# Kernel optimization log

Hardware: AMD Instinct MI355X
Metric: run time of the kernel (lower is better)

The kernel has to match this reference:

```python
import jax, jax.numpy as jnp
import numpy as np

EMBED_DIM = 512
NUM_HEADS = 8
QKV_DIM = 64
MS_HIDDEN = 16
COST_DIMS = 1
SCORES_DIMS = COST_DIMS + 1  # dot-product score + cost-mat score


def setup_inputs() -> dict:
    key = jax.random.key(0)
    ks = jax.random.split(key, 12)
    B, R, C = 8, 256, 256
    row_emb = jax.random.normal(ks[0], (B, R, EMBED_DIM), dtype=jnp.float32)
    col_emb = jax.random.normal(ks[1], (B, C, EMBED_DIM), dtype=jnp.float32)
    cost_mat = jax.random.uniform(ks[2], (B, R, C, COST_DIMS), dtype=jnp.float32)
    attn_mask = jax.random.randint(ks[3], (B, R, C), 0, 2).astype(jnp.bool_)
    # learned params (stored [in, out]; torch Linear applies x @ W.T)
    s = 1.0 / np.sqrt(EMBED_DIM)
    Wq = jax.random.uniform(ks[4], (EMBED_DIM, NUM_HEADS * QKV_DIM), minval=-s, maxval=s)
    Wk = jax.random.uniform(ks[5], (EMBED_DIM, NUM_HEADS * QKV_DIM), minval=-s, maxval=s)
    Wv = jax.random.uniform(ks[6], (EMBED_DIM, NUM_HEADS * QKV_DIM), minval=-s, maxval=s)
    Wo = jax.random.uniform(ks[7], (EMBED_DIM, EMBED_DIM), minval=-s, maxval=s)
    m1 = np.sqrt(1.0 / SCORES_DIMS)
    m2 = np.sqrt(1.0 / MS_HIDDEN)
    W1 = jax.random.uniform(ks[8], (SCORES_DIMS * NUM_HEADS, MS_HIDDEN * NUM_HEADS), minval=-m1, maxval=m1)
    W2 = jax.random.uniform(ks[9], (MS_HIDDEN * NUM_HEADS, NUM_HEADS), minval=-m2, maxval=m2)
    alpha = jnp.ones((1, NUM_HEADS, 1, 1, 1), dtype=jnp.float32)
    return {"row_emb": row_emb, "col_emb": col_emb, "cost_mat": cost_mat,
            "attn_mask": attn_mask, "Wq": Wq, "Wk": Wk, "Wv": Wv, "Wo": Wo,
            "W1": W1, "W2": W2, "alpha": alpha}


def reference(row_emb, col_emb, cost_mat, attn_mask, Wq, Wk, Wv, Wo, W1, W2, alpha):
    B, R, E = row_emb.shape
    C = col_emb.shape[1]
    H, D = NUM_HEADS, QKV_DIM
    norm = 1.0 / jnp.sqrt(jnp.asarray(D, row_emb.dtype))
    # projections -> (b, h, s, d)
    q = (row_emb @ Wq).reshape(B, R, H, D).transpose(0, 2, 1, 3)
    k = (col_emb @ Wk).reshape(B, C, H, D).transpose(0, 2, 1, 3)
    v = (col_emb @ Wv).reshape(B, C, H, D).transpose(0, 2, 1, 3)
    dot = norm * jnp.einsum('bhrd,bhcd->bhrc', q, k)  # (B,H,R,C)
    # mixed-score MLP: concat dot score with alpha-scaled cost-mat score
    cm = alpha * cost_mat[:, None]                    # (B,H,R,C,COST_DIMS)
    scores = jnp.concatenate([dot[..., None], cm], axis=-1)  # (B,H,R,C,S)
    s = scores.transpose(0, 2, 3, 1, 4).reshape(B, R, C, H * SCORES_DIMS)
    mixed = jax.nn.relu(s @ W1) @ W2                  # (B,R,C,H)
    logits = mixed.transpose(0, 3, 1, 2)              # (B,H,R,C)
    # masked softmax (rows fully masked -> zero weights)
    mask = attn_mask[:, None]                         # (B,1,R,C)
    all_masked = jnp.all(mask, axis=-1, keepdims=True)
    logits = jnp.where(mask, -jnp.inf, logits)
    weights = jax.nn.softmax(logits, axis=-1)
    weights = jnp.where(all_masked, 0.0, weights)
    out = jnp.einsum('bhrc,bhcd->bhrd', weights, v)   # (B,H,R,D)
    out = out.transpose(0, 2, 1, 3).reshape(B, R, H * D)
    return out @ Wo
```

## Files before the change

### kernel.cpp

```cpp
#include <hip/hip_runtime.h>
#include <hip/hip_bf16.h>

#define B_ 8
#define R_ 256
#define C_ 256
#define H_ 8
#define D_ 64

typedef __attribute__((ext_vector_type(8))) short s8v;
typedef __attribute__((ext_vector_type(4))) short s4v;
typedef __attribute__((ext_vector_type(4))) float f4v;

static __device__ __forceinline__ unsigned short f2b(float x) {
    __hip_bfloat16 h = __float2bfloat16(x);
    return *reinterpret_cast<unsigned short*>(&h);
}
static __device__ __forceinline__ float b2f(unsigned short u) {
    union { unsigned int i; float f; } c;
    c.i = (unsigned int)u << 16;
    return c.f;
}

__global__ __launch_bounds__(256) void prep(
    const float* __restrict__ re, const float* __restrict__ ce,
    const float* __restrict__ W1, const float* __restrict__ W2,
    const float* __restrict__ alpha,
    const float* __restrict__ Wq, const float* __restrict__ Wk,
    const float* __restrict__ Wv, const float* __restrict__ Wo,
    unsigned short* __restrict__ reb, unsigned short* __restrict__ ceb,
    unsigned short* __restrict__ w1af, unsigned short* __restrict__ w2af,
    unsigned short* __restrict__ wqt, unsigned short* __restrict__ wkt,
    unsigned short* __restrict__ wvt, unsigned short* __restrict__ wot)
{
    __shared__ unsigned short ldsT[64][68];
    if (blockIdx.x >= 2048) {
        const int bb = blockIdx.x - 2048;
        const int which = bb >> 6;
        const float* W = which == 0 ? Wq : which == 1 ? Wk : which == 2 ? Wv : Wo;
        unsigned short* WT = which == 0 ? wqt : which == 1 ? wkt : which == 2 ? wvt : wot;
        const int k0 = (bb & 7) * 64;
        const int n0 = ((bb >> 3) & 7) * 64;
        const int tt = threadIdx.x;
        const int rn = tt & 15;
        const int rk = tt >> 4;
        #pragma unroll
        for (int i = 0; i < 4; ++i) {
            const int kk = rk + 16 * i;
            const float4 v = *(const float4*)&W[(size_t)(k0 + kk) * 512 + n0 + rn * 4];
            ldsT[rn * 4 + 0][kk] = f2b(v.x);
            ldsT[rn * 4 + 1][kk] = f2b(v.y);
            ldsT[rn * 4 + 2][kk] = f2b(v.z);
            ldsT[rn * 4 + 3][kk] = f2b(v.w);
        }
        __syncthreads();
        #pragma unroll
        for (int i = 0; i < 4; ++i) {
            const int nn = rk + 16 * i;
            const s4v r = *(const s4v*)&ldsT[nn][rn * 4];
            *(s4v*)&WT[(size_t)(n0 + nn) * 512 + k0 + rn * 4] = r;
        }
        return;
    }

    const int t = blockIdx.x * 256 + threadIdx.x;
    {
        float2 v = *(const float2*)&re[(size_t)t * 2];
        reb[t * 2]     = f2b(v.x);
        reb[t * 2 + 1] = f2b(v.y);
        float2 w = *(const float2*)&ce[(size_t)t * 2];
        ceb[t * 2]     = f2b(w.x);
        ceb[t * 2 + 1] = f2b(w.y);
    }
    if (blockIdx.x == 0) {
        const int l = threadIdx.x;
        for (int q = 0; q < 16; ++q) {
            const int idx = l * 16 + q;
            const int kk = idx & 7, lane = (idx >> 3) & 63, n = idx >> 9;
            const int j = n * 16 + (lane & 15);
            const int s = 8 * (lane >> 4) + kk;
            float val = 0.f;
            if (s < 16) {
                val = W1[(2 * (s >> 1)) * 128 + j];
            } else if (s < 18) {
                for (int h = 0; h < 8; ++h)
                    val += alpha[h] * W1[(2 * h + 1) * 128 + j];
            }
            w1af[idx] = f2b(val);
        }
        for (int q = 0; q < 8; ++q) {
            const int idx = l * 8 + q;
            const int kk = idx & 7, lane = (idx >> 3) & 63, kc = idx >> 9;
            const int h = lane & 15, g = lane >> 4;
            const int phi = 16 * (2 * kc + (kk >> 2)) + 4 * g + (kk & 3);
            w2af[idx] = f2b(h < 8 ? W2[phi * 8 + h] : 0.f);
        }
    }
}

__global__ __launch_bounds__(256) void gemm_qkv(
    const unsigned short* __restrict__ reb, const unsigned short* __restrict__ ceb,
    const unsigned short* __restrict__ wqt, const unsigned short* __restrict__ wkt,
    const unsigned short* __restrict__ wvt,
    unsigned short* __restrict__ Qb, unsigned short* __restrict__ Kb,
    unsigned short* __restrict__ VT)
{
    const int z = blockIdx.z;
    const unsigned short* A;
    const unsigned short* Bm;
    int Ar0, Br0;
    if (z == 0)      { A = reb; Bm = wqt; Ar0 = blockIdx.x * 64; Br0 = blockIdx.y * 64; }
    else if (z == 1) { A = ceb; Bm = wkt; Ar0 = blockIdx.x * 64; Br0 = blockIdx.y * 64; }
    else             { A = wvt; Bm = ceb; Ar0 = blockIdx.y * 64; Br0 = blockIdx.x * 64; }

    const int t = threadIdx.x, lane = t & 63, wave = t >> 6;
    const int row0 = Ar0 + (wave >> 1) * 32;
    const int col0 = Br0 + (wave & 1) * 32;
    const int lr = lane & 15, ko = (lane >> 4) * 8;

    const unsigned short* Ap0 = A + (size_t)(row0 + lr) * 512 + ko;
    const unsigned short* Ap1 = Ap0 + 16 * 512;
    const unsigned short* Bp0 = Bm + (size_t)(col0 + lr) * 512 + ko;
    const unsigned short* Bp1 = Bp0 + 16 * 512;

    f4v acc[2][2] = {};
    s8v a0 = *(const s8v*)Ap0;
    s8v a1 = *(const s8v*)Ap1;
    s8v b0 = *(const s8v*)Bp0;
    s8v b1 = *(const s8v*)Bp1;
    #pragma unroll
    for (int k0 = 0; k0 < 512; k0 += 32) {
        const s8v ca0 = a0, ca1 = a1, cb0 = b0, cb1 = b1;
        if (k0 + 32 < 512) {
            a0 = *(const s8v*)(Ap0 + k0 + 32);
            a1 = *(const s8v*)(Ap1 + k0 + 32);
            b0 = *(const s8v*)(Bp0 + k0 + 32);
            b1 = *(const s8v*)(Bp1 + k0 + 32);
        }
        acc[0][0] = __builtin_amdgcn_mfma_f32_16x16x32_bf16(ca0, cb0, acc[0][0], 0, 0, 0);
        acc[0][1] = __builtin_amdgcn_mfma_f32_16x16x32_bf16(ca0, cb1, acc[0][1], 0, 0, 0);
        acc[1][0] = __builtin_amdgcn_mfma_f32_16x16x32_bf16(ca1, cb0, acc[1][0], 0, 0, 0);
        acc[1][1] = __builtin_amdgcn_mfma_f32_16x16x32_bf16(ca1, cb1, acc[1][1], 0, 0, 0);
    }

    const float sc = (z == 0) ? 0.125f : 1.0f;
    const int rbase = (lane >> 4) * 4;
    #pragma unroll
    for (int i = 0; i < 2; ++i)
        #pragma unroll
        for (int j = 0; j < 2; ++j)
            #pragma unroll
            for (int reg = 0; reg < 4; ++reg) {
                const int rowIdx = row0 + i * 16 + rbase + reg;
                const int colIdx = col0 + j * 16 + lr;
                const unsigned short v = f2b(acc[i][j][reg] * sc);
                if (z == 0) {
                    Qb[(size_t)rowIdx * 512 + colIdx] = v;
                } else if (z == 1) {
                    const int b = rowIdx >> 8, c = rowIdx & 255;
                    const int h = colIdx >> 6, d = colIdx & 63;
                    Kb[(((size_t)b * 8 + h) * 256 + c) * 64 + d] = v;
                } else {
                    const int h = rowIdx >> 6, d = rowIdx & 63;
                    const int b = colIdx >> 8, c = colIdx & 255;
                    VT[(((size_t)b * 8 + h) * 64 + d) * 256 + c] = v;
                }
            }
}

__global__ __launch_bounds__(256) void gemm_out(
    const unsigned short* __restrict__ OHb, const unsigned short* __restrict__ wot,
    float* __restrict__ out)
{
    const int t = threadIdx.x, lane = t & 63, wave = t >> 6;
    const int row0 = blockIdx.x * 32 + (wave & 1) * 16;
    const int col0 = blockIdx.y * 64 + (wave >> 1) * 32;
    const int lr = lane & 15, ko = (lane >> 4) * 8;

    const unsigned short* Ap0 = OHb + (size_t)(row0 + lr) * 512 + ko;
    const unsigned short* Bp0 = wot + (size_t)(col0 + lr) * 512 + ko;
    const unsigned short* Bp1 = Bp0 + 16 * 512;

    f4v acc[2] = {};
    s8v a0 = *(const s8v*)Ap0;
    s8v b0 = *(const s8v*)Bp0;
    s8v b1 = *(const s8v*)Bp1;
    #pragma unroll
    for (int k0 = 0; k0 < 512; k0 += 32) {
        const s8v ca0 = a0, cb0 = b0, cb1 = b1;
        if (k0 + 32 < 512) {
            a0 = *(const s8v*)(Ap0 + k0 + 32);
            b0 = *(const s8v*)(Bp0 + k0 + 32);
            b1 = *(const s8v*)(Bp1 + k0 + 32);
        }
        acc[0] = __builtin_amdgcn_mfma_f32_16x16x32_bf16(ca0, cb0, acc[0], 0, 0, 0);
        acc[1] = __builtin_amdgcn_mfma_f32_16x16x32_bf16(ca0, cb1, acc[1], 0, 0, 0);
    }

    const int rbase = (lane >> 4) * 4;
    #pragma unroll
    for (int j = 0; j < 2; ++j)
        #pragma unroll
        for (int reg = 0; reg < 4; ++reg)
            out[(size_t)(row0 + rbase + reg) * 512 + col0 + j * 16 + lr] = acc[j][reg];
}

__global__ __launch_bounds__(1024) void attn_fused(
    const unsigned short* __restrict__ Qb,
    const unsigned short* __restrict__ Kb,
    const unsigned short* __restrict__ VT,
    const float* __restrict__ cost,
    const int* __restrict__ mask,
    const unsigned short* __restrict__ w1af,
    const unsigned short* __restrict__ w2af,
    unsigned short* __restrict__ OHb)
{
    __shared__ unsigned short dotb[8][256][16];
    __shared__ unsigned short w_t3[8][8][264];
    __shared__ unsigned short ws1[4096];
    __shared__ unsigned short ws2[2048];

    const int t    = threadIdx.x;
    const int lane = t & 63;
    const int w    = t >> 6;
    const int li   = lane & 15;
    const int g    = lane >> 4;
    const int b    = blockIdx.y;
    const int r0   = blockIdx.x * 8;

    const int h  = w & 7;
    const int hf = w >> 3;

    if (t < 512) ((s8v*)ws1)[t] = ((const s8v*)w1af)[t];
    else if (t < 768) ((s8v*)ws2)[t - 512] = ((const s8v*)w2af)[t - 512];

    const int rB  = w & 7;
    const int ct0 = hf * 8;
    float costv[8];
    {
        const float* costRow = cost + ((size_t)b * R_ + r0 + rB) * 256;
        #pragma unroll
        for (int i = 0; i < 8; ++i)
            costv[i] = costRow[(ct0 + i) * 16 + li];
    }
    int mkp[4][4];
    #pragma unroll
    for (int p = 0; p < 4; ++p) {
        const int idx = w * 4 + p;
        const int* maskRow = mask + ((size_t)b * R_ + r0 + (idx >> 3)) * 256;
        #pragma unroll
        for (int i = 0; i < 4; ++i)
            mkp[p][i] = maskRow[lane + 64 * i];
    }

    {
        const int rr = lane & 7;
        const int ko = g * 8;
        const unsigned short* Qp = Qb + ((size_t)b * R_ + r0 + rr) * 512 + h * 64 + ko;
        const s8v a0 = *(const s8v*)Qp;
        const s8v a1 = *(const s8v*)(Qp + 32);
        const unsigned short* Kp = Kb + (((size_t)b * 8 + h) * 256) * 64;
        #pragma unroll
        for (int c8 = 0; c8 < 8; ++c8) {
            const int ct = ct0 + c8;
            const unsigned short* Bp = Kp + (size_t)(ct * 16 + li) * 64 + ko;
            const s8v b0 = *(const s8v*)Bp;
            const s8v b1v = *(const s8v*)(Bp + 32);
            f4v acc = __builtin_amdgcn_mfma_f32_16x16x32_bf16(a0, b0, (f4v){0.f,0.f,0.f,0.f}, 0, 0, 0);
            acc = __builtin_amdgcn_mfma_f32_16x16x32_bf16(a1, b1v, acc, 0, 0, 0);
            if (g < 2) {
                const int c = ct * 16 + li;
                #pragma unroll
                for (int reg = 0; reg < 4; ++reg) {
                    const float x = acc[reg];
                    const unsigned short hi = f2b(x);
                    const unsigned short lo = f2b(x - b2f(hi));
                    *(unsigned int*)&dotb[4 * g + reg][c][2 * h] =
                        (unsigned int)hi | ((unsigned int)lo << 16);
                }
            }
        }
    }
    __syncthreads();

    s8v b1r[8];
    #pragma unroll
    for (int i = 0; i < 8; ++i) {
        const int c = (ct0 + i) * 16 + li;
        b1r[i] = *(const s8v*)&dotb[rB][c][(g & 1) * 8];
    }
    __syncthreads();

    {
        float* lplane = (float*)&dotb[rB][0][0];
        #pragma unroll
        for (int i = 0; i < 8; ++i) {
            const int c = (ct0 + i) * 16 + li;
            s8v b1;
            {
                const float cv = costv[i];
                const unsigned short chi = f2b(cv);
                const unsigned short clo = f2b(cv - b2f(chi));
                if (g < 2) {
                    b1 = b1r[i];
                } else if (g == 2) {
                    s8v bc = {0, 0, 0, 0, 0, 0, 0, 0};
                    bc[0] = (short)chi; bc[1] = (short)clo;
                    b1 = bc;
                } else {
                    s8v bz = {0, 0, 0, 0, 0, 0, 0, 0};
                    b1 = bz;
                }
            }
            unsigned int pk[16];
            #pragma unroll
            for (int n = 0; n < 8; ++n) {
                const s8v w1A = *(const s8v*)&ws1[(n * 64 + lane) * 8];
                f4v acc = __builtin_amdgcn_mfma_f32_16x16x32_bf16(
                    w1A, b1, (f4v){0.f,0.f,0.f,0.f}, 0, 0, 0);
                const float a0 = fmaxf(acc[0], 0.f), a1 = fmaxf(acc[1], 0.f);
                const float a2 = fmaxf(acc[2], 0.f), a3 = fmaxf(acc[3], 0.f);
                pk[2 * n]     = (unsigned int)f2b(a0) | ((unsigned int)f2b(a1) << 16);
                pk[2 * n + 1] = (unsigned int)f2b(a2) | ((unsigned int)f2b(a3) << 16);
            }
            f4v acc2 = (f4v){0.f, 0.f, 0.f, 0.f};
            #pragma unroll
            for (int kc = 0; kc < 4; ++kc) {
                const s8v w2A = *(const s8v*)&ws2[(kc * 64 + lane) * 8];
                union { s8v v; unsigned int u[4]; } bb;
                bb.u[0] = pk[4 * kc + 0];
                bb.u[1] = pk[4 * kc + 1];
                bb.u[2] = pk[4 * kc + 2];
                bb.u[3] = pk[4 * kc + 3];
                acc2 = __builtin_amdgcn_mfma_f32_16x16x32_bf16(w2A, bb.v, acc2, 0, 0, 0);
            }
            if (g < 2) {
                #pragma unroll
                for (int reg = 0; reg < 4; ++reg)
                    lplane[(4 * g + reg) * 256 + c] = acc2[reg];
            }
        }
    }
    __syncthreads();

    {
        #pragma unroll
        for (int p = 0; p < 4; ++p) {
            const int idx = w * 4 + p;
            const int r = idx >> 3, hh = idx & 7;
            const float* lplane = (const float*)&dotb[r][0][0];
            float v[4];
            #pragma unroll
            for (int i = 0; i < 4; ++i)
                v[i] = lplane[hh * 256 + lane + 64 * i];
            #pragma unroll
            for (int i = 0; i < 4; ++i)
                v[i] = mkp[p][i] ? -INFINITY : v[i];
            float mx = fmaxf(fmaxf(v[0], v[1]), fmaxf(v[2], v[3]));
            #pragma unroll
            for (int off = 32; off >= 1; off >>= 1)
                mx = fmaxf(mx, __shfl_xor(mx, off));
            float e[4];
            #pragma unroll
            for (int i = 0; i < 4; ++i)
                e[i] = mkp[p][i] ? 0.f : __expf(v[i] - mx);
            float sm = e[0] + e[1] + e[2] + e[3];
            #pragma unroll
            for (int off = 32; off >= 1; off >>= 1)
                sm += __shfl_xor(sm, off);
            const float inv = sm > 0.f ? 1.0f / sm : 0.f;
            #pragma unroll
            for (int i = 0; i < 4; ++i)
                w_t3[hh][r][lane + 64 * i] = f2b(e[i] * inv);
        }
    }
    __syncthreads();

    {
        s8v bfr[8];
        #pragma unroll
        for (int kt = 0; kt < 8; ++kt)
            bfr[kt] = *(const s8v*)&w_t3[h][li & 7][kt * 32 + g * 8];
        const unsigned short* Vp = VT + (((size_t)b * 8 + h) * 64) * 256;
        #pragma unroll
        for (int d2 = 0; d2 < 2; ++d2) {
            const int dt = hf * 2 + d2;
            const unsigned short* Ap = Vp + (size_t)(dt * 16 + li) * 256 + g * 8;
            f4v acc = (f4v){0.f, 0.f, 0.f, 0.f};
            #pragma unroll
            for (int kt = 0; kt < 8; ++kt)
                acc = __builtin_amdgcn_mfma_f32_16x16x32_bf16(
                    *(const s8v*)(Ap + kt * 32), bfr[kt], acc, 0, 0, 0);
            if (li < 8) {
                s4v o;
                o[0] = (short)f2b(acc[0]);
                o[1] = (short)f2b(acc[1]);
                o[2] = (short)f2b(acc[2]);
                o[3] = (short)f2b(acc[3]);
                *(s4v*)&OHb[((size_t)b * R_ + r0 + li) * 512 + h * 64 + dt * 16 + 4 * g] = o;
            }
        }
    }
}

extern "C" void kernel_launch(void* const* d_in, const int* in_sizes, int n_in,
                              void* d_out, int out_size, void* d_ws, size_t ws_size,
                              hipStream_t stream)
{
    const float* row_emb = (const float*)d_in[0];
    const float* col_emb = (const float*)d_in[1];
    const float* cost    = (const float*)d_in[2];
    const int*   mask    = (const int*)d_in[3];
    const float* Wq = (const float*)d_in[4];
    const float* Wk = (const float*)d_in[5];
    const float* Wv = (const float*)d_in[6];
    const float* Wo = (const float*)d_in[7];
    const float* W1 = (const float*)d_in[8];
    const float* W2 = (const float*)d_in[9];
    const float* alpha = (const float*)d_in[10];
    float* out = (float*)d_out;

    unsigned short* base = (unsigned short*)d_ws;
    unsigned short* Qb   = base;
    unsigned short* Kb   = base + 1048576;
    unsigned short* VT   = base + 2097152;
    unsigned short* OHb  = base + 3145728;
    unsigned short* reb  = base + 4194304;
    unsigned short* ceb  = base + 5242880;
    unsigned short* wqt  = base + 6291456;
    unsigned short* wkt  = base + 6553600;
    unsigned short* wvt  = base + 6815744;
    unsigned short* wot  = base + 7077888;
    unsigned short* w1af = base + 7340032;
    unsigned short* w2af = base + 7344128;

    prep<<<2304, 256, 0, stream>>>(row_emb, col_emb, W1, W2, alpha,
                                   Wq, Wk, Wv, Wo,
                                   reb, ceb, w1af, w2af, wqt, wkt, wvt, wot);
    gemm_qkv<<<dim3(32, 8, 3), 256, 0, stream>>>(reb, ceb, wqt, wkt, wvt,
                                                 Qb, Kb, VT);
    attn_fused<<<dim3(32, 8), 1024, 0, stream>>>(Qb, Kb, VT, cost, mask,
                                                 w1af, w2af, OHb);
    gemm_out<<<dim3(64, 8), 256, 0, stream>>>(OHb, wot, out);
}
```

Measured before the change: 83.38 us.

## Merge all four kernels into one cooperative persistent kernel with grid syncs

Replaces the prep, QKV GEMM, attention and output GEMM launches with one cooperative kernel of 256 blocks of 1024 threads, with stages separated by grid-wide syncs. Each stage's work is remapped onto the fixed grid by wave id. This is meant to remove the per-launch overhead and the inter-kernel gaps. In exchange, the GEMM stages run with only 256 large blocks, so occupancy is lower. The large LDS footprint of the attention stage also limits residency, and the grid barriers add their own cost.

```diff
diff --git a/kernel.cpp b/kernel.cpp
--- a/kernel.cpp
+++ b/kernel.cpp
@@ -1,5 +1,8 @@
 #include <hip/hip_runtime.h>
 #include <hip/hip_bf16.h>
+#include <hip/hip_cooperative_groups.h>
+
+namespace cg = cooperative_groups;
 
 #define B_ 8
 #define R_ 256
@@ -21,31 +24,62 @@
     return c.f;
 }
 
-__global__ __launch_bounds__(256) void prep(
+__global__ __launch_bounds__(1024) void mega(
     const float* __restrict__ re, const float* __restrict__ ce,
+    const float* __restrict__ cost, const int* __restrict__ mask,
+    const float* __restrict__ Wq, const float* __restrict__ Wk,
+    const float* __restrict__ Wv, const float* __restrict__ Wo,
     const float* __restrict__ W1, const float* __restrict__ W2,
     const float* __restrict__ alpha,
-    const float* __restrict__ Wq, const float* __restrict__ Wk,
-    const float* __restrict__ Wv, const float* __restrict__ Wo,
     unsigned short* __restrict__ reb, unsigned short* __restrict__ ceb,
     unsigned short* __restrict__ w1af, unsigned short* __restrict__ w2af,
     unsigned short* __restrict__ wqt, unsigned short* __restrict__ wkt,
-    unsigned short* __restrict__ wvt, unsigned short* __restrict__ wot)
+    unsigned short* __restrict__ wvt, unsigned short* __restrict__ wot,
+    unsigned short* __restrict__ Qb, unsigned short* __restrict__ Kb,
+    unsigned short* __restrict__ VT, unsigned short* __restrict__ OHb,
+    float* __restrict__ out)
 {
+    __shared__ unsigned short dotb[8][256][16];
+    __shared__ unsigned short w_t3[8][8][264];
+    __shared__ unsigned short ws1[4096];
+    __shared__ unsigned short ws2[2048];
     __shared__ unsigned short ldsT[64][68];
-    if (blockIdx.x >= 2048) {
-        const int bb = blockIdx.x - 2048;
-        const int which = bb >> 6;
+
+    const int t    = threadIdx.x;
+    const int lane = t & 63;
+    const int w    = t >> 6;
+    const int li   = lane & 15;
+    const int g    = lane >> 4;
+    const int bid  = blockIdx.y * 32 + blockIdx.x;
+    const int wid  = bid * 16 + w;
+    cg::grid_group gg = cg::this_grid();
+
+    {
+        const size_t gi = (size_t)(bid * 1024 + t) * 4;
+        {
+            const float4 v = *(const float4*)&re[gi];
+            s4v rv;
+            rv[0] = (short)f2b(v.x); rv[1] = (short)f2b(v.y);
+            rv[2] = (short)f2b(v.z); rv[3] = (short)f2b(v.w);
+            *(s4v*)&reb[gi] = rv;
+            const float4 u = *(const float4*)&ce[gi];
+            s4v cv;
+            cv[0] = (short)f2b(u.x); cv[1] = (short)f2b(u.y);
+            cv[2] = (short)f2b(u.z); cv[3] = (short)f2b(u.w);
+            *(s4v*)&ceb[gi] = cv;
+        }
+        const int which = bid >> 6;
         const float* W = which == 0 ? Wq : which == 1 ? Wk : which == 2 ? Wv : Wo;
-        unsigned short* WT = which == 0 ? wqt : which == 1 ? wkt : which == 2 ? wvt : wot;
-        const int k0 = (bb & 7) * 64;
-        const int n0 = ((bb >> 3) & 7) * 64;
-        const int tt = threadIdx.x;
-        const int rn = tt & 15;
-        const int rk = tt >> 4;
-        #pragma unroll
-        for (int i = 0; i < 4; ++i) {
-            const int kk = rk + 16 * i;
+        unsigned short* WT = which == 0 ? wqt : which == 1 ? wkt
+                           : which == 2 ? wvt : wot;
+        const int tile = bid & 63;
+        const int k0 = (tile & 7) * 64;
+        const int n0 = (tile >> 3) * 64;
+        const int rn = t & 15;
+        const int rk = (t >> 4) & 15;
+        const int qi = t >> 8;
+        {
+            const int kk = rk + 16 * qi;
             const float4 v = *(const float4*)&W[(size_t)(k0 + kk) * 512 + n0 + rn * 4];
             ldsT[rn * 4 + 0][kk] = f2b(v.x);
             ldsT[rn * 4 + 1][kk] = f2b(v.y);
@@ -53,180 +87,108 @@
             ldsT[rn * 4 + 3][kk] = f2b(v.w);
         }
         __syncthreads();
-        #pragma unroll
-        for (int i = 0; i < 4; ++i) {
-            const int nn = rk + 16 * i;
+        {
+            const int nn = rk + 16 * qi;
             const s4v r = *(const s4v*)&ldsT[nn][rn * 4];
             *(s4v*)&WT[(size_t)(n0 + nn) * 512 + k0 + rn * 4] = r;
         }
-        return;
-    }
-
-    const int t = blockIdx.x * 256 + threadIdx.x;
-    {
-        float2 v = *(const float2*)&re[(size_t)t * 2];
-        reb[t * 2]     = f2b(v.x);
-        reb[t * 2 + 1] = f2b(v.y);
-        float2 w = *(const float2*)&ce[(size_t)t * 2];
-        ceb[t * 2]     = f2b(w.x);
-        ceb[t * 2 + 1] = f2b(w.y);
-    }
-    if (blockIdx.x == 0) {
-        const int l = threadIdx.x;
-        for (int q = 0; q < 16; ++q) {
-            const int idx = l * 16 + q;
-            const int kk = idx & 7, lane = (idx >> 3) & 63, n = idx >> 9;
-            const int j = n * 16 + (lane & 15);
-            const int s = 8 * (lane >> 4) + kk;
-            float val = 0.f;
-            if (s < 16) {
-                val = W1[(2 * (s >> 1)) * 128 + j];
-            } else if (s < 18) {
-                for (int h = 0; h < 8; ++h)
-                    val += alpha[h] * W1[(2 * h + 1) * 128 + j];
-            }
-            w1af[idx] = f2b(val);
-        }
-        for (int q = 0; q < 8; ++q) {
-            const int idx = l * 8 + q;
-            const int kk = idx & 7, lane = (idx >> 3) & 63, kc = idx >> 9;
-            const int h = lane & 15, g = lane >> 4;
-            const int phi = 16 * (2 * kc + (kk >> 2)) + 4 * g + (kk & 3);
-            w2af[idx] = f2b(h < 8 ? W2[phi * 8 + h] : 0.f);
-        }
-    }
-}
-
-__global__ __launch_bounds__(256) void gemm_qkv(
-    const unsigned short* __restrict__ reb, const unsigned short* __restrict__ ceb,
-    const unsigned short* __restrict__ wqt, const unsigned short* __restrict__ wkt,
-    const unsigned short* __restrict__ wvt,
-    unsigned short* __restrict__ Qb, unsigned short* __restrict__ Kb,
-    unsigned short* __restrict__ VT)
-{
-    const int z = blockIdx.z;
-    const unsigned short* A;
-    const unsigned short* Bm;
-    int Ar0, Br0;
-    if (z == 0)      { A = reb; Bm = wqt; Ar0 = blockIdx.x * 64; Br0 = blockIdx.y * 64; }
-    else if (z == 1) { A = ceb; Bm = wkt; Ar0 = blockIdx.x * 64; Br0 = blockIdx.y * 64; }
-    else             { A = wvt; Bm = ceb; Ar0 = blockIdx.y * 64; Br0 = blockIdx.x * 64; }
-
-    const int t = threadIdx.x, lane = t & 63, wave = t >> 6;
-    const int row0 = Ar0 + (wave >> 1) * 32;
-    const int col0 = Br0 + (wave & 1) * 32;
-    const int lr = lane & 15, ko = (lane >> 4) * 8;
-
-    const unsigned short* Ap0 = A + (size_t)(row0 + lr) * 512 + ko;
-    const unsigned short* Ap1 = Ap0 + 16 * 512;
-    const unsigned short* Bp0 = Bm + (size_t)(col0 + lr) * 512 + ko;
-    const unsigned short* Bp1 = Bp0 + 16 * 512;
-
-    f4v acc[2][2] = {};
-    s8v a0 = *(const s8v*)Ap0;
-    s8v a1 = *(const s8v*)Ap1;
-    s8v b0 = *(const s8v*)Bp0;
-    s8v b1 = *(const s8v*)Bp1;
-    #pragma unroll
-    for (int k0 = 0; k0 < 512; k0 += 32) {
-        const s8v ca0 = a0, ca1 = a1, cb0 = b0, cb1 = b1;
-        if (k0 + 32 < 512) {
-            a0 = *(const s8v*)(Ap0 + k0 + 32);
-            a1 = *(const s8v*)(Ap1 + k0 + 32);
-            b0 = *(const s8v*)(Bp0 + k0 + 32);
-            b1 = *(const s8v*)(Bp1 + k0 + 32);
-        }
-        acc[0][0] = __builtin_amdgcn_mfma_f32_16x16x32_bf16(ca0, cb0, acc[0][0], 0, 0, 0);
-        acc[0][1] = __builtin_amdgcn_mfma_f32_16x16x32_bf16(ca0, cb1, acc[0][1], 0, 0, 0);
-        acc[1][0] = __builtin_amdgcn_mfma_f32_16x16x32_bf16(ca1, cb0, acc[1][0], 0, 0, 0);
-        acc[1][1] = __builtin_amdgcn_mfma_f32_16x16x32_bf16(ca1, cb1, acc[1][1], 0, 0, 0);
-    }
-
-    const float sc = (z == 0) ? 0.125f : 1.0f;
-    const int rbase = (lane >> 4) * 4;
-    #pragma unroll
-    for (int i = 0; i < 2; ++i)
-        #pragma unroll
-        for (int j = 0; j < 2; ++j)
-            #pragma unroll
-            for (int reg = 0; reg < 4; ++reg) {
-                const int rowIdx = row0 + i * 16 + rbase + reg;
-                const int colIdx = col0 + j * 16 + lr;
-                const unsigned short v = f2b(acc[i][j][reg] * sc);
-                if (z == 0) {
-                    Qb[(size_t)rowIdx * 512 + colIdx] = v;
-                } else if (z == 1) {
-                    const int b = rowIdx >> 8, c = rowIdx & 255;
-                    const int h = colIdx >> 6, d = colIdx & 63;
-                    Kb[(((size_t)b * 8 + h) * 256 + c) * 64 + d] = v;
-                } else {
-                    const int h = rowIdx >> 6, d = rowIdx & 63;
-                    const int b = colIdx >> 8, c = colIdx & 255;
-                    VT[(((size_t)b * 8 + h) * 64 + d) * 256 + c] = v;
+        if (bid == 0 && t < 256) {
+            const int l = t;
+            for (int q = 0; q < 16; ++q) {
+                const int idx = l * 16 + q;
+                const int kk = idx & 7, ln = (idx >> 3) & 63, n = idx >> 9;
+                const int j = n * 16 + (ln & 15);
+                const int s = 8 * (ln >> 4) + kk;
+                float val = 0.f;
+                if (s < 16) {
+                    val = W1[(2 * (s >> 1)) * 128 + j];
+                } else if (s < 18) {
+                    for (int hh = 0; hh < 8; ++hh)
+                        val += alpha[hh] * W1[(2 * hh + 1) * 128 + j];
                 }
-            }
-}
-
-__global__ __launch_bounds__(256) void gemm_out(
-    const unsigned short* __restrict__ OHb, const unsigned short* __restrict__ wot,
-    float* __restrict__ out)
-{
-    const int t = threadIdx.x, lane = t & 63, wave = t >> 6;
-    const int row0 = blockIdx.x * 32 + (wave & 1) * 16;
-    const int col0 = blockIdx.y * 64 + (wave >> 1) * 32;
-    const int lr = lane & 15, ko = (lane >> 4) * 8;
-
-    const unsigned short* Ap0 = OHb + (size_t)(row0 + lr) * 512 + ko;
-    const unsigned short* Bp0 = wot + (size_t)(col0 + lr) * 512 + ko;
-    const unsigned short* Bp1 = Bp0 + 16 * 512;
-
-    f4v acc[2] = {};
-    s8v a0 = *(const s8v*)Ap0;
-    s8v b0 = *(const s8v*)Bp0;
-    s8v b1 = *(const s8v*)Bp1;
-    #pragma unroll
-    for (int k0 = 0; k0 < 512; k0 += 32) {
-        const s8v ca0 = a0, cb0 = b0, cb1 = b1;
-        if (k0 + 32 < 512) {
-            a0 = *(const s8v*)(Ap0 + k0 + 32);
-            b0 = *(const s8v*)(Bp0 + k0 + 32);
-            b1 = *(const s8v*)(Bp1 + k0 + 32);
-        }
-        acc[0] = __builtin_amdgcn_mfma_f32_16x16x32_bf16(ca0, cb0, acc[0], 0, 0, 0);
-        acc[1] = __builtin_amdgcn_mfma_f32_16x16x32_bf16(ca0, cb1, acc[1], 0, 0, 0);
-    }
-
-    const int rbase = (lane >> 4) * 4;
-    #pragma unroll
-    for (int j = 0; j < 2; ++j)
-        #pragma unroll
-        for (int reg = 0; reg < 4; ++reg)
-            out[(size_t)(row0 + rbase + reg) * 512 + col0 + j * 16 + lr] = acc[j][reg];
-}
-
-__global__ __launch_bounds__(1024) void attn_fused(
-    const unsigned short* __restrict__ Qb,
-    const unsigned short* __restrict__ Kb,
-    const unsigned short* __restrict__ VT,
-    const float* __restrict__ cost,
-    const int* __restrict__ mask,
-    const unsigned short* __restrict__ w1af,
-    const unsigned short* __restrict__ w2af,
-    unsigned short* __restrict__ OHb)
-{
-    __shared__ unsigned short dotb[8][256][16];
-    __shared__ unsigned short w_t3[8][8][264];
-    __shared__ unsigned short ws1[4096];
-    __shared__ unsigned short ws2[2048];
-
-    const int t    = threadIdx.x;
-    const int lane = t & 63;
-    const int w    = t >> 6;
-    const int li   = lane & 15;
-    const int g    = lane >> 4;
-    const int b    = blockIdx.y;
-    const int r0   = blockIdx.x * 8;
-
+                w1af[idx] = f2b(val);
+            }
+            for (int q = 0; q < 8; ++q) {
+                const int idx = l * 8 + q;
+                const int kk = idx & 7, ln = (idx >> 3) & 63, kc = idx >> 9;
+                const int hh = ln & 15, gg2 = ln >> 4;
+                const int phi = 16 * (2 * kc + (kk >> 2)) + 4 * gg2 + (kk & 3);
+                w2af[idx] = f2b(hh < 8 ? W2[phi * 8 + hh] : 0.f);
+            }
+        }
+    }
+    gg.sync();
+
+    if (wid < 3072) {
+        const int z = wid >> 10;
+        const int rem = wid & 1023;
+        const int tile = rem >> 2;
+        const int wv = rem & 3;
+        const int x = tile >> 3;
+        const int y = tile & 7;
+        const unsigned short* A;
+        const unsigned short* Bm;
+        int Ar0, Br0;
+        if (z == 0)      { A = reb; Bm = wqt; Ar0 = x * 64; Br0 = y * 64; }
+        else if (z == 1) { A = ceb; Bm = wkt; Ar0 = x * 64; Br0 = y * 64; }
+        else             { A = wvt; Bm = ceb; Ar0 = y * 64; Br0 = x * 64; }
+        const int row0 = Ar0 + (wv >> 1) * 32;
+        const int col0 = Br0 + (wv & 1) * 32;
+        const int lr = li, ko = g * 8;
+
+        const unsigned short* Ap0 = A + (size_t)(row0 + lr) * 512 + ko;
+        const unsigned short* Ap1 = Ap0 + 16 * 512;
+        const unsigned short* Bp0 = Bm + (size_t)(col0 + lr) * 512 + ko;
+        const unsigned short* Bp1 = Bp0 + 16 * 512;
+
+        f4v acc[2][2] = {};
+        s8v a0 = *(const s8v*)Ap0;
+        s8v a1 = *(const s8v*)Ap1;
+        s8v b0 = *(const s8v*)Bp0;
+        s8v b1 = *(const s8v*)Bp1;
+        #pragma unroll
+        for (int k0 = 0; k0 < 512; k0 += 32) {
+            const s8v ca0 = a0, ca1 = a1, cb0 = b0, cb1 = b1;
+            if (k0 + 32 < 512) {
+                a0 = *(const s8v*)(Ap0 + k0 + 32);
+                a1 = *(const s8v*)(Ap1 + k0 + 32);
+                b0 = *(const s8v*)(Bp0 + k0 + 32);
+                b1 = *(const s8v*)(Bp1 + k0 + 32);
+            }
+            acc[0][0] = __builtin_amdgcn_mfma_f32_16x16x32_bf16(ca0, cb0, acc[0][0], 0, 0, 0);
+            acc[0][1] = __builtin_amdgcn_mfma_f32_16x16x32_bf16(ca0, cb1, acc[0][1], 0, 0, 0);
+            acc[1][0] = __builtin_amdgcn_mfma_f32_16x16x32_bf16(ca1, cb0, acc[1][0], 0, 0, 0);
+            acc[1][1] = __builtin_amdgcn_mfma_f32_16x16x32_bf16(ca1, cb1, acc[1][1], 0, 0, 0);
+        }
+
+        const float sc = (z == 0) ? 0.125f : 1.0f;
+        const int rbase = g * 4;
+        #pragma unroll
+        for (int i = 0; i < 2; ++i)
+            #pragma unroll
+            for (int j = 0; j < 2; ++j)
+                #pragma unroll
+                for (int reg = 0; reg < 4; ++reg) {
+                    const int rowIdx = row0 + i * 16 + rbase + reg;
+                    const int colIdx = col0 + j * 16 + lr;
+                    const unsigned short v = f2b(acc[i][j][reg] * sc);
+                    if (z == 0) {
+                        Qb[(size_t)rowIdx * 512 + colIdx] = v;
+                    } else if (z == 1) {
+                        const int b = rowIdx >> 8, c = rowIdx & 255;
+                        const int hh = colIdx >> 6, d = colIdx & 63;
+                        Kb[(((size_t)b * 8 + hh) * 256 + c) * 64 + d] = v;
+                    } else {
+                        const int hh = rowIdx >> 6, d = rowIdx & 63;
+                        const int b = colIdx >> 8, c = colIdx & 255;
+                        VT[(((size_t)b * 8 + hh) * 64 + d) * 256 + c] = v;
+                    }
+                }
+    }
+    gg.sync();
+
+    const int b  = blockIdx.y;
+    const int r0 = blockIdx.x * 8;
     const int h  = w & 7;
     const int hf = w >> 3;
 
@@ -400,16 +362,54 @@
             }
         }
     }
+    gg.sync();
+
+    if (wid < 2048) {
+        const int bx = wid >> 5;
+        const int rem = wid & 31;
+        const int by = rem >> 2;
+        const int wv = rem & 3;
+        const int row0 = bx * 32 + (wv & 1) * 16;
+        const int col0 = by * 64 + (wv >> 1) * 32;
+        const int lr = li, ko = g * 8;
+
+        const unsigned short* Ap0 = OHb + (size_t)(row0 + lr) * 512 + ko;
+        const unsigned short* Bp0 = wot + (size_t)(col0 + lr) * 512 + ko;
+        const unsigned short* Bp1 = Bp0 + 16 * 512;
+
+        f4v acc[2] = {};
+        s8v a0 = *(const s8v*)Ap0;
+        s8v b0 = *(const s8v*)Bp0;
+        s8v b1 = *(const s8v*)Bp1;
+        #pragma unroll
+        for (int k0 = 0; k0 < 512; k0 += 32) {
+            const s8v ca0 = a0, cb0 = b0, cb1 = b1;
+            if (k0 + 32 < 512) {
+                a0 = *(const s8v*)(Ap0 + k0 + 32);
+                b0 = *(const s8v*)(Bp0 + k0 + 32);
+                b1 = *(const s8v*)(Bp1 + k0 + 32);
+            }
+            acc[0] = __builtin_amdgcn_mfma_f32_16x16x32_bf16(ca0, cb0, acc[0], 0, 0, 0);
+            acc[1] = __builtin_amdgcn_mfma_f32_16x16x32_bf16(ca0, cb1, acc[1], 0, 0, 0);
+        }
+
+        const int rbase = g * 4;
+        #pragma unroll
+        for (int j = 0; j < 2; ++j)
+            #pragma unroll
+            for (int reg = 0; reg < 4; ++reg)
+                out[(size_t)(row0 + rbase + reg) * 512 + col0 + j * 16 + lr] = acc[j][reg];
+    }
 }
 
 extern "C" void kernel_launch(void* const* d_in, const int* in_sizes, int n_in,
                               void* d_out, int out_size, void* d_ws, size_t ws_size,
                               hipStream_t stream)
 {
-    const float* row_emb = (const float*)d_in[0];
-    const float* col_emb = (const float*)d_in[1];
-    const float* cost    = (const float*)d_in[2];
-    const int*   mask    = (const int*)d_in[3];
+    const float* re   = (const float*)d_in[0];
+    const float* ce   = (const float*)d_in[1];
+    const float* cost = (const float*)d_in[2];
+    const int*   mask = (const int*)d_in[3];
     const float* Wq = (const float*)d_in[4];
     const float* Wk = (const float*)d_in[5];
     const float* Wv = (const float*)d_in[6];
@@ -433,12 +433,14 @@
     unsigned short* w1af = base + 7340032;
     unsigned short* w2af = base + 7344128;
 
-    prep<<<2304, 256, 0, stream>>>(row_emb, col_emb, W1, W2, alpha,
-                                   Wq, Wk, Wv, Wo,
-                                   reb, ceb, w1af, w2af, wqt, wkt, wvt, wot);
-    gemm_qkv<<<dim3(32, 8, 3), 256, 0, stream>>>(reb, ceb, wqt, wkt, wvt,
-                                                 Qb, Kb, VT);
-    attn_fused<<<dim3(32, 8), 1024, 0, stream>>>(Qb, Kb, VT, cost, mask,
-                                                 w1af, w2af, OHb);
-    gemm_out<<<dim3(64, 8), 256, 0, stream>>>(OHb, wot, out);
+    void* args[] = {
+        (void*)&re, (void*)&ce, (void*)&cost, (void*)&mask,
+        (void*)&Wq, (void*)&Wk, (void*)&Wv, (void*)&Wo,
+        (void*)&W1, (void*)&W2, (void*)&alpha,
+        (void*)&reb, (void*)&ceb, (void*)&w1af, (void*)&w2af,
+        (void*)&wqt, (void*)&wkt, (void*)&wvt, (void*)&wot,
+        (void*)&Qb, (void*)&Kb, (void*)&VT, (void*)&OHb, (void*)&out
+    };
+    hipLaunchCooperativeKernel((void*)mega, dim3(32, 8, 1), dim3(1024, 1, 1),
+                               args, 0, stream);
 }
```

Result: slower. 199.1 us (+138.8%).
